# Performance work log

Hardware: AMD Instinct MI355X
Metric: run time of the kernel (lower is better)

Reference implementation:

```python
import jax, jax.numpy as jnp
import numpy as np

# MLABlock dims (from __init__ defaults / chosen init_kwargs)
B, S, D = 2, 2048, 2048
H = 16
NOPE, ROPE, VD = 128, 64, 128
KVR = 512
NE, TOPK = 12, 4
EI, SEI = 1024, 2048
THETA = 10000.0
MSCALE = 1.0
EPS = 1e-6


def setup_inputs() -> dict:
    key = jax.random.key(0)
    ks = jax.random.split(key, 14)
    w = lambda k, shp: jax.random.normal(k, shp, jnp.float32) * 0.02
    return {
        "x": jax.random.normal(ks[0], (B, S, D), jnp.float32),
        "start_pos": 0,
        "norm_w": jnp.ones((D,), jnp.float32),
        "wq": w(ks[1], (H * (NOPE + ROPE), D)),
        "wkv_a": w(ks[2], (KVR + ROPE, D)),
        "kv_norm_w": jnp.ones((KVR,), jnp.float32),
        "wkv_b": w(ks[3], (H * (NOPE + VD), KVR)),
        "wo": w(ks[4], (D, H * VD)),
        "gate_w": w(ks[5], (NE, D)),
        "gate_bias": w(ks[6], (NE,)),
        "w1": w(ks[7], (NE, EI, D)),
        "w2": w(ks[8], (NE, D, EI)),
        "w3": w(ks[9], (NE, EI, D)),
        "sw1": w(ks[10], (SEI, D)),
        "sw2": w(ks[11], (D, SEI)),
        "sw3": w(ks[12], (SEI, D)),
    }


def _rms(v, w):
    return v * jax.lax.rsqrt(jnp.mean(v * v, -1, keepdims=True) + EPS) * w


def reference(x, start_pos, norm_w, wq, wkv_a, kv_norm_w, wkv_b, wo,
              gate_w, gate_bias, w1, w2, w3, sw1, sw2, sw3):
    b, s, d = x.shape
    # ---- MLA attention sub-layer ----
    h = _rms(x, norm_w)
    q = (h @ wq.T).reshape(b, s, H, NOPE + ROPE)
    q_nope, q_pe = q[..., :NOPE], q[..., NOPE:]
    kv = h @ wkv_a.T                      # [b,s,KVR+ROPE]
    kv_lat, k_pe = kv[..., :KVR], kv[..., KVR:]
    # rotary embedding (interleaved pairs), positions start_pos..start_pos+s
    pos = jnp.arange(s, dtype=jnp.float32) + start_pos
    inv = 1.0 / (THETA ** (jnp.arange(0, ROPE, 2, dtype=jnp.float32) / ROPE))
    ang = pos[:, None] * inv              # [s, ROPE/2]
    cos = jnp.cos(ang)[None, :, None, :]
    sin = jnp.sin(ang)[None, :, None, :]
    def rot(t):                           # t: [b,s,h,ROPE]
        t1, t2 = t[..., 0::2], t[..., 1::2]
        return jnp.stack([t1 * cos - t2 * sin, t1 * sin + t2 * cos], -1).reshape(t.shape)
    q_pe = rot(q_pe)
    k_pe = rot(k_pe[:, :, None, :])       # [b,s,1,ROPE] shared across heads
    kv_lat = _rms(kv_lat, kv_norm_w)
    kvb = (kv_lat @ wkv_b.T).reshape(b, s, H, NOPE + VD)
    k_nope, v = kvb[..., :NOPE], kvb[..., NOPE:]
    k = jnp.concatenate([k_nope, jnp.broadcast_to(k_pe, (b, s, H, ROPE))], -1)
    qf = jnp.concatenate([q_nope, q_pe], -1)
    scale = MSCALE * (NOPE + ROPE) ** -0.5
    mask = jnp.triu(jnp.full((s, s), -1e9, x.dtype), 1)  # causal
    scores = jnp.einsum('bqhd,bkhd->bhqk', qf, k) * scale + mask
    attn = jax.nn.softmax(scores, -1)
    o = jnp.einsum('bhqk,bkhd->bqhd', attn, v).reshape(b, s, H * VD) @ wo.T
    first = o + x
    # ---- MoE sub-layer (shared self.norm reused) ----
    h2 = _rms(first, norm_w)
    g_scores = jax.nn.sigmoid(h2 @ gate_w.T)             # [b,s,NE]
    _, idx = jax.lax.top_k(g_scores + gate_bias, TOPK)   # adaptive-bias selection
    gw = jnp.take_along_axis(g_scores, idx, -1)          # weights from raw scores
    gw = gw / jnp.sum(gw, -1, keepdims=True)
    out = (jax.nn.silu(h2 @ sw1.T) * (h2 @ sw3.T)) @ sw2.T  # shared expert
    for e in range(NE):                                  # fixed small expert set
        we = jnp.sum(jnp.where(idx == e, gw, 0.0), -1)   # [b,s]
        ye = (jax.nn.silu(h2 @ w1[e].T) * (h2 @ w3[e].T)) @ w2[e].T
        out = out + we[..., None] * ye
    return out + first
```

## Files before the change

### kernel.cpp

```cpp
#include <hip/hip_runtime.h>
#include <cstdint>
#include <cstddef>
#include <cmath>

#define DI __device__ __forceinline__
typedef float f32x4 __attribute__((ext_vector_type(4)));
typedef __bf16 bf16x8 __attribute__((ext_vector_type(8)));
typedef unsigned short u16;
typedef unsigned int u32;

static constexpr int TKN = 4096, SEQ = 2048, DIM = 2048, NH = 16;

DI u16 f2bf(float f) {
  union { float f; u32 u; } v; v.f = f;
  u32 r = v.u + 0x7fffu + ((v.u >> 16) & 1u);
  return (u16)(r >> 16);
}
DI float bf2f(u16 h) {
  union { u32 u; float f; } v; v.u = ((u32)h) << 16;
  return v.f;
}
DI f32x4 mfma16(bf16x8 a, bf16x8 b, f32x4 c) {
  return __builtin_amdgcn_mfma_f32_16x16x32_bf16(a, b, c, 0, 0, 0);
}
DI void gld16(const u16* g, u16* l) {
  __builtin_amdgcn_global_load_lds((const __attribute__((address_space(1))) u32*)g,
                                   (__attribute__((address_space(3))) u32*)l, 16, 0, 0);
}

enum { EF_F32 = 0, EF_BF16 = 1, EF_RES = 2, EF_KV = 3, EF_SILU = 4, EF_ATOM = 5, EF_QROPE = 6 };
enum { AM_DIR = 0, AM_LIST = 1, AM_OFF = 2, AM_TIL = 3 };

template<int EPI, int AMODE, int NSEG>
__global__ __launch_bounds__(256)
void gemm_f(const u16* __restrict__ A, const u16* __restrict__ B, void* __restrict__ C,
            int M, int N, int K, size_t apl, size_t bpl,
            const int* __restrict__ list, const int* __restrict__ basep,
            const int* __restrict__ counts,
            const void* __restrict__ aux, const float* __restrict__ gws,
            u16* __restrict__ kd0, u16* __restrict__ kd1, u16* __restrict__ vT,
            const float* __restrict__ cosT, const int* __restrict__ tb)
{
  constexpr int BM = 128, BK = 64;
  __shared__ __align__(16) u16 As[BM * BK];
  __shared__ __align__(16) u16 Bs[BM * BK];
  int rowbase = 0;
  int m0, n0;
  if (AMODE == AM_TIL) {
    int ntile = N >> 7;
    int u = blockIdx.x / ntile;
    if (u >= tb[12]) return;
    n0 = (blockIdx.x - u * ntile) << 7;
    int e = 0;
    #pragma unroll
    for (int k = 0; k < 11; k++) if (tb[k + 1] <= u) e = k + 1;
    M = counts[e];
    rowbase = basep[e];
    m0 = (u - tb[e]) << 7;
    B += (size_t)e * (size_t)N * K;
  } else if (AMODE != AM_DIR) {
    int z = blockIdx.z;
    M = counts[z];
    rowbase = basep[z];
    B += (size_t)z * (size_t)N * K;
    m0 = blockIdx.x * BM; n0 = blockIdx.y * BM;
    if (m0 >= M) return;
  } else {
    m0 = blockIdx.x * BM; n0 = blockIdx.y * BM;
    if (m0 >= M) return;
  }
  int tid = threadIdx.x, lane = tid & 63, wid = tid >> 6;
  int wm = (wid >> 1) * 64, wn = (wid & 1) * 64;
  int lr = lane & 15, lk = (lane >> 4) * 8;

  const u16* asrc[4];
  const u16* bsrc[4];
  int l8 = lane >> 3, c8 = ((lane & 7) ^ l8) * 8;
  #pragma unroll
  for (int i = 0; i < 4; i++) {
    int chunk = wid * 4 + i;
    int ra = m0 + chunk * 8 + l8;
    size_t rowidx;
    if (AMODE == AM_LIST)      rowidx = (size_t)list[rowbase + (ra < M ? ra : 0)];
    else if (AMODE == AM_OFF || AMODE == AM_TIL)
                               rowidx = (size_t)(rowbase + (ra < M ? ra : 0));
    else                       rowidx = (size_t)ra;
    asrc[i] = A + rowidx * (size_t)K + c8;
    int rb = n0 + chunk * 8 + l8;
    if (rb >= N) rb = N - 1;
    bsrc[i] = B + (size_t)rb * K + c8;
  }

  f32x4 acc[4][4] = {};
  int sw = lr & 7;
  #pragma unroll 1
  for (int s = 0; s < NSEG; s++) {
    int sa = (s == 4) ? 2 : (s & 1);
    int sb = (s == 5) ? 2 : ((s >> 1) & 1);
    size_t ao = (size_t)sa * apl, bo = (size_t)sb * bpl;
    for (int kt = 0; kt < K; kt += BK) {
      #pragma unroll
      for (int i = 0; i < 4; i++) {
        gld16(asrc[i] + ao + kt, &As[(wid * 4 + i) * 512]);
        gld16(bsrc[i] + bo + kt, &Bs[(wid * 4 + i) * 512]);
      }
      __syncthreads();
      #pragma unroll
      for (int ko = 0; ko < BK; ko += 32) {
        bf16x8 af[4], bv[4];
        int sl = ((((ko + lk) >> 3) ^ sw) << 3);
        #pragma unroll
        for (int i = 0; i < 4; i++)
          af[i] = *(const bf16x8*)(&As[(wm + i * 16 + lr) * 64 + sl]);
        #pragma unroll
        for (int j = 0; j < 4; j++)
          bv[j] = *(const bf16x8*)(&Bs[(wn + j * 16 + lr) * 64 + sl]);
        #pragma unroll
        for (int i = 0; i < 4; i++)
          #pragma unroll
          for (int j = 0; j < 4; j++)
            acc[i][j] = mfma16(af[i], bv[j], acc[i][j]);
      }
      __syncthreads();
    }
  }

  int og = (lane >> 4) * 4;
  if (EPI == EF_KV) {
    if (((n0 >> 7) & 1) == 0) {
      #pragma unroll
      for (int i = 0; i < 4; i++)
        #pragma unroll
        for (int p = 0; p < 4; p++) {
          int r = m0 + wm + i * 16 + og + p;
          #pragma unroll
          for (int j = 0; j < 4; j++) {
            int c = n0 + wn + j * 16 + lr;
            float v = acc[i][j][p];
            int hd = c >> 8, cc = c & 127;
            u16 b0 = f2bf(v);
            u16 b1 = f2bf(v - bf2f(b0));
            size_t base = ((size_t)r * NH + hd) * 128 + cc;
            kd0[base] = b0; kd1[base] = b1;
          }
        }
    } else {
      constexpr size_t VPL = (size_t)32 * 128 * 2048;
      #pragma unroll
      for (int i = 0; i < 4; i++) {
        int r0 = m0 + wm + i * 16 + og;
        int bb = r0 >> 11, ss = r0 & 2047;
        #pragma unroll
        for (int j = 0; j < 4; j++) {
          int c = n0 + wn + j * 16 + lr;
          int hd = c >> 8, ccv = c & 127;
          ushort4 q0, q1, q2;
          #pragma unroll
          for (int p = 0; p < 4; p++) {
            float v = acc[i][j][p];
            u16 b0 = f2bf(v);
            float r1 = v - bf2f(b0);
            u16 b1 = f2bf(r1);
            u16 b2 = f2bf(r1 - bf2f(b1));
            ((u16*)&q0)[p] = b0; ((u16*)&q1)[p] = b1; ((u16*)&q2)[p] = b2;
          }
          size_t vb = ((size_t)((bb * 16 + hd) * 128 + ccv)) * 2048 + ss;
          *(ushort4*)(vT + vb) = q0;
          *(ushort4*)(vT + VPL + vb) = q1;
          *(ushort4*)(vT + 2 * VPL + vb) = q2;
        }
      }
    }
  } else {
    #pragma unroll
    for (int i = 0; i < 4; i++)
      #pragma unroll
      for (int p = 0; p < 4; p++) {
        int r = m0 + wm + i * 16 + og + p;
        if (EPI != EF_QROPE) { if (r >= M) continue; }
        size_t outr = (AMODE == AM_DIR) ? (size_t)r : (size_t)(rowbase + r);
        #pragma unroll
        for (int j = 0; j < 4; j++) {
          int c = n0 + wn + j * 16 + lr;
          float v = acc[i][j][p];
          if (EPI == EF_F32) {
            if (c < N) ((float*)C)[outr * N + c] = v;
          } else if (EPI == EF_BF16) {
            ((u16*)C)[outr * N + c] = f2bf(v);
          } else if (EPI == EF_RES) {
            ((float*)C)[outr * N + c] = v + ((const float*)aux)[outr * N + c];
          } else if (EPI == EF_SILU) {
            float t = bf2f(((const u16*)aux)[outr * N + c]);
            float sg = t / (1.f + __expf(-t));
            ((u16*)C)[outr * N + c] = f2bf(sg * v);
          } else if (EPI == EF_ATOM) {
            int tok = list[outr];
            float w = gws[outr];
            atomicAdd((float*)C + (size_t)tok * N + c, w * v);
          } else if (EPI == EF_QROPE) {
            int wi = c % 192;
            float vo = v;
            if (wi >= 128) {
              float part = __shfl_xor(v, 1);
              int jj = (wi - 128) >> 1;
              int srow = r & (SEQ - 1);
              float cs = cosT[srow * 32 + jj];
              float sn = ((const float*)aux)[srow * 32 + jj];
              vo = (c & 1) ? (part * sn + v * cs) : (v * cs - part * sn);
            }
            u16 b0 = f2bf(vo);
            u16 b1 = f2bf(vo - bf2f(b0));
            kd0[outr * (size_t)N + c] = b0;
            kd1[outr * (size_t)N + c] = b1;
          }
        }
      }
  }
}

__global__ __launch_bounds__(256)
void attn3(const u16* __restrict__ q0p, const u16* __restrict__ q1p,
           const u16* __restrict__ k0p, const u16* __restrict__ k1p,
           const u16* __restrict__ kp0, const u16* __restrict__ kp1,
           const u16* __restrict__ vT, u16* __restrict__ o0, float scale)
{
  constexpr int KLD = 200, VLD = 40, PLD = 36;
  constexpr size_t VPL = (size_t)32 * 128 * 2048;
  constexpr size_t OPL = (size_t)TKN * DIM;
  __shared__ __align__(16) u16 Ks[2][32 * KLD];
  __shared__ __align__(16) u16 Vt[3][128 * VLD];
  __shared__ __align__(16) float Ps[4][16 * PLD];

  int bh = blockIdx.y;
  int b = bh >> 4, h = bh & 15;
  int tid = threadIdx.x, lane = tid & 63, wid = tid >> 6;
  int lr = lane & 15, lg = lane >> 4, lk = lg * 8;
  size_t tbase = (size_t)b * SEQ;
  const u16* vbase = vT + (size_t)bh * 128 * 2048;

  for (int half = 0; half < 2; half++) {
    int qt = half ? (31 - (int)blockIdx.x) : (int)blockIdx.x;
    int q0r = qt * 64;
    bf16x8 qf[2][6];
    {
      size_t qoff = (tbase + q0r + wid * 16 + lr) * (size_t)3072 + h * 192;
      #pragma unroll
      for (int kc = 0; kc < 6; kc++) {
        qf[0][kc] = *(const bf16x8*)(q0p + qoff + kc * 32 + lk);
        qf[1][kc] = *(const bf16x8*)(q1p + qoff + kc * 32 + lk);
      }
    }
    f32x4 oacc[8] = {};
    float mrow[4], lrow[4];
    #pragma unroll
    for (int p = 0; p < 4; p++) { mrow[p] = -1e30f; lrow[p] = 0.f; }

    int nkt = 2 * qt + 2;
    for (int kt = 0; kt < nkt; kt++) {
      __syncthreads();
      int kr0 = kt * 32;
      #pragma unroll
      for (int p = 0; p < 2; p++) {
        const u16* knp = p ? k1p : k0p;
        const u16* kpp = p ? kp1 : kp0;
        #pragma unroll
        for (int i = 0; i < 2; i++) {
          int vv = tid + i * 256, r = vv >> 4, cc8 = (vv & 15) * 8;
          int4 d = *(const int4*)(knp + ((tbase + kr0 + r) * (size_t)NH + h) * 128 + cc8);
          *(int4*)(&Ks[p][r * KLD + cc8]) = d;
        }
        {
          int r = tid >> 3, cc8 = (tid & 7) * 8;
          int4 d = *(const int4*)(kpp + (tbase + kr0 + r) * (size_t)64 + cc8);
          *(int4*)(&Ks[p][r * KLD + 128 + cc8]) = d;
        }
      }
      #pragma unroll
      for (int p = 0; p < 3; p++) {
        #pragma unroll
        for (int i = 0; i < 2; i++) {
          int vv = tid + i * 256, d = vv >> 2, cc8 = (vv & 3) * 8;
          int4 dd = *(const int4*)(vbase + p * VPL + (size_t)d * 2048 + kr0 + cc8);
          *(int4*)(&Vt[p][d * VLD + cc8]) = dd;
        }
      }
      __syncthreads();

      f32x4 sacc[2] = {};
      #pragma unroll
      for (int j = 0; j < 2; j++)
        #pragma unroll
        for (int kc = 0; kc < 6; kc++) {
          bf16x8 kf0 = *(const bf16x8*)(&Ks[0][(j * 16 + lr) * KLD + kc * 32 + lk]);
          bf16x8 kf1 = *(const bf16x8*)(&Ks[1][(j * 16 + lr) * KLD + kc * 32 + lk]);
          f32x4 t = sacc[j];
          t = mfma16(qf[0][kc], kf0, t);
          t = mfma16(qf[1][kc], kf0, t);
          t = mfma16(qf[0][kc], kf1, t);
          sacc[j] = t;
        }

      bool tail = (kt >= 2 * qt);
      float fsc[4];
      #pragma unroll
      for (int p = 0; p < 4; p++) {
        float s0 = sacc[0][p] * scale, s1 = sacc[1][p] * scale;
        if (tail) {
          int qrow = q0r + wid * 16 + lg * 4 + p;
          if (kr0 + lr > qrow) s0 = -1e30f;
          if (kr0 + 16 + lr > qrow) s1 = -1e30f;
        }
        float mx = fmaxf(s0, s1);
        #pragma unroll
        for (int off = 1; off < 16; off <<= 1) mx = fmaxf(mx, __shfl_xor(mx, off));
        float mnew = fmaxf(mrow[p], mx);
        fsc[p] = __expf(mrow[p] - mnew);
        float e0 = __expf(s0 - mnew), e1 = __expf(s1 - mnew);
        float ssum = e0 + e1;
        #pragma unroll
        for (int off = 1; off < 16; off <<= 1) ssum += __shfl_xor(ssum, off);
        lrow[p] = lrow[p] * fsc[p] + ssum;
        mrow[p] = mnew;
        Ps[wid][(lg * 4 + p) * PLD + lr] = e0;
        Ps[wid][(lg * 4 + p) * PLD + 16 + lr] = e1;
      }
      #pragma unroll
      for (int jf = 0; jf < 8; jf++) {
        f32x4 t = oacc[jf];
        t[0] *= fsc[0]; t[1] *= fsc[1]; t[2] *= fsc[2]; t[3] *= fsc[3];
        oacc[jf] = t;
      }

      f32x4 pva = *(const f32x4*)(&Ps[wid][lr * PLD + lk]);
      f32x4 pvb = *(const f32x4*)(&Ps[wid][lr * PLD + lk + 4]);
      union { u16 us[8]; bf16x8 v; } pa0u, pa1u;
      #pragma unroll
      for (int e = 0; e < 4; e++) {
        float va = pva[e];
        u16 b0 = f2bf(va); pa0u.us[e] = b0; pa1u.us[e] = f2bf(va - bf2f(b0));
        float vb = pvb[e];
        u16 c0 = f2bf(vb); pa0u.us[4 + e] = c0; pa1u.us[4 + e] = f2bf(vb - bf2f(c0));
      }

      #pragma unroll
      for (int jf = 0; jf < 8; jf++) {
        bf16x8 vf0 = *(const bf16x8*)(&Vt[0][(jf * 16 + lr) * VLD + lk]);
        bf16x8 vf1 = *(const bf16x8*)(&Vt[1][(jf * 16 + lr) * VLD + lk]);
        bf16x8 vf2 = *(const bf16x8*)(&Vt[2][(jf * 16 + lr) * VLD + lk]);
        f32x4 t = oacc[jf];
        t = mfma16(pa0u.v, vf0, t);
        t = mfma16(pa1u.v, vf0, t);
        t = mfma16(pa0u.v, vf1, t);
        t = mfma16(pa1u.v, vf1, t);
        t = mfma16(pa0u.v, vf2, t);
        oacc[jf] = t;
      }
    }

    #pragma unroll
    for (int p = 0; p < 4; p++) {
      float inv = 1.f / lrow[p];
      int qrow = q0r + wid * 16 + lg * 4 + p;
      size_t base = (tbase + qrow) * (size_t)DIM + h * 128;
      #pragma unroll
      for (int jf = 0; jf < 8; jf++) {
        float val = oacc[jf][p] * inv;
        u16 b0 = f2bf(val);
        float r1 = val - bf2f(b0);
        u16 b1 = f2bf(r1);
        u16 b2 = f2bf(r1 - bf2f(b1));
        size_t idx = base + jf * 16 + lr;
        o0[idx] = b0; o0[OPL + idx] = b1; o0[2 * OPL + idx] = b2;
      }
    }
  }
}

__global__ __launch_bounds__(256)
void rmsnorm3(const float* __restrict__ x, const float* __restrict__ w, u16* __restrict__ out)
{
  __shared__ float sred[4];
  constexpr size_t PL = (size_t)TKN * DIM;
  int t = blockIdx.x, tid = threadIdx.x;
  const float* xp = x + (size_t)t * DIM;
  float vals[8], ss = 0.f;
  #pragma unroll
  for (int i = 0; i < 8; i++) { float v = xp[tid + i * 256]; vals[i] = v; ss += v * v; }
  #pragma unroll
  for (int off = 32; off > 0; off >>= 1) ss += __shfl_xor(ss, off);
  if ((tid & 63) == 0) sred[tid >> 6] = ss;
  __syncthreads();
  ss = sred[0] + sred[1] + sred[2] + sred[3];
  float rstd = 1.f / sqrtf(ss / (float)DIM + 1e-6f);
  #pragma unroll
  for (int i = 0; i < 8; i++) {
    int d = tid + i * 256;
    float v = vals[i] * rstd * w[d];
    u16 b0 = f2bf(v);
    float r1 = v - bf2f(b0);
    u16 b1 = f2bf(r1);
    u16 b2 = f2bf(r1 - bf2f(b1));
    size_t o = (size_t)t * DIM + d;
    out[o] = b0; out[PL + o] = b1; out[2 * PL + o] = b2;
  }
}

__global__ __launch_bounds__(256)
void split3(const float* __restrict__ src, u16* __restrict__ dst, size_t n, size_t pl)
{
  size_t i0 = ((size_t)blockIdx.x * 256 + threadIdx.x) * 4;
  size_t stride = (size_t)gridDim.x * 1024;
  for (size_t i = i0; i < n; i += stride) {
    float4 d = *(const float4*)(src + i);
    ushort4 b0, b1, b2; float r;
    b0.x = f2bf(d.x); r = d.x - bf2f(b0.x); b1.x = f2bf(r); b2.x = f2bf(r - bf2f(b1.x));
    b0.y = f2bf(d.y); r = d.y - bf2f(b0.y); b1.y = f2bf(r); b2.y = f2bf(r - bf2f(b1.y));
    b0.z = f2bf(d.z); r = d.z - bf2f(b0.z); b1.z = f2bf(r); b2.z = f2bf(r - bf2f(b1.z));
    b0.w = f2bf(d.w); r = d.w - bf2f(b0.w); b1.w = f2bf(r); b2.w = f2bf(r - bf2f(b1.w));
    *(ushort4*)(dst + i) = b0;
    *(ushort4*)(dst + pl + i) = b1;
    *(ushort4*)(dst + 2 * pl + i) = b2;
  }
}

__global__ __launch_bounds__(256)
void cvt1(const float* __restrict__ src, u16* __restrict__ dst, size_t n)
{
  size_t i0 = ((size_t)blockIdx.x * 256 + threadIdx.x) * 4;
  size_t stride = (size_t)gridDim.x * 1024;
  for (size_t i = i0; i < n; i += stride) {
    float4 d = *(const float4*)(src + i);
    ushort4 b;
    b.x = f2bf(d.x); b.y = f2bf(d.y); b.z = f2bf(d.z); b.w = f2bf(d.w);
    *(ushort4*)(dst + i) = b;
  }
}

__global__ __launch_bounds__(256)
void gather_h2(const u16* __restrict__ h2, const int* __restrict__ list,
               u16* __restrict__ h2g)
{
  int slot = blockIdx.x;
  int tok = list[slot];
  int4 d = *(const int4*)(h2 + (size_t)tok * DIM + threadIdx.x * 8);
  *(int4*)(h2g + (size_t)slot * DIM + threadIdx.x * 8) = d;
}

__global__ __launch_bounds__(256)
void kv_split(const float* __restrict__ kvraw, const float* __restrict__ kvw,
              u16* __restrict__ c0, u16* __restrict__ kp0, u16* __restrict__ kp1,
              const float* __restrict__ cosT, const float* __restrict__ sinT)
{
  __shared__ float sred[4];
  constexpr size_t CPL = (size_t)TKN * 512;
  int t = blockIdx.x, tid = threadIdx.x;
  const float* xp = kvraw + (size_t)t * 576;
  float v0 = xp[tid], v1 = xp[tid + 256];
  float ss = v0 * v0 + v1 * v1;
  #pragma unroll
  for (int off = 32; off > 0; off >>= 1) ss += __shfl_xor(ss, off);
  if ((tid & 63) == 0) sred[tid >> 6] = ss;
  __syncthreads();
  ss = sred[0] + sred[1] + sred[2] + sred[3];
  float rstd = 1.f / sqrtf(ss / 512.f + 1e-6f);
  #pragma unroll
  for (int half = 0; half < 2; half++) {
    float v = (half ? v1 : v0) * rstd * kvw[tid + half * 256];
    u16 b0 = f2bf(v);
    float r1 = v - bf2f(b0);
    u16 b1 = f2bf(r1);
    u16 b2 = f2bf(r1 - bf2f(b1));
    size_t o = (size_t)t * 512 + tid + half * 256;
    c0[o] = b0; c0[CPL + o] = b1; c0[2 * CPL + o] = b2;
  }
  if (tid < 32) {
    int srow = t & (SEQ - 1);
    float a = xp[512 + tid * 2], bb = xp[512 + tid * 2 + 1];
    float cs = cosT[srow * 32 + tid], sn = sinT[srow * 32 + tid];
    float ra = a * cs - bb * sn, rb = a * sn + bb * cs;
    u16 a0 = f2bf(ra), a1 = f2bf(ra - bf2f(a0));
    u16 c0b = f2bf(rb), c1 = f2bf(rb - bf2f(c0b));
    kp0[(size_t)t * 64 + tid * 2] = a0;     kp1[(size_t)t * 64 + tid * 2] = a1;
    kp0[(size_t)t * 64 + tid * 2 + 1] = c0b; kp1[(size_t)t * 64 + tid * 2 + 1] = c1;
  }
}

__global__ __launch_bounds__(256)
void rope_table(float* __restrict__ cosT, float* __restrict__ sinT, const int* __restrict__ sp)
{
  int i = blockIdx.x * 256 + threadIdx.x;
  if (i >= SEQ * 32) return;
  int j = i & 31, srow = i >> 5;
  float pos = (float)(srow + sp[0]);
  float inv = powf(10000.f, -(float)(2 * j) / 64.f);
  cosT[i] = cosf(pos * inv);
  sinT[i] = sinf(pos * inv);
}

__global__ __launch_bounds__(256)
void gate_topk(const float* __restrict__ first, const float* __restrict__ nw,
               const float* __restrict__ gwm, const float* __restrict__ gbias,
               int* __restrict__ idx, float* __restrict__ gw4, int* __restrict__ counts,
               u16* __restrict__ h2out)
{
  __shared__ float sred[4];
  __shared__ float sacc[12][4];
  int t = blockIdx.x, tid = threadIdx.x;
  const float* xp = first + (size_t)t * DIM;
  float vals[8], ss = 0.f;
  #pragma unroll
  for (int i = 0; i < 8; i++) { float v = xp[tid + i * 256]; vals[i] = v; ss += v * v; }
  #pragma unroll
  for (int off = 32; off > 0; off >>= 1) ss += __shfl_xor(ss, off);
  if ((tid & 63) == 0) sred[tid >> 6] = ss;
  __syncthreads();
  ss = sred[0] + sred[1] + sred[2] + sred[3];
  float rstd = 1.f / sqrtf(ss / (float)DIM + 1e-6f);
  float acc[12];
  #pragma unroll
  for (int e = 0; e < 12; e++) acc[e] = 0.f;
  #pragma unroll
  for (int i = 0; i < 8; i++) {
    int d = tid + i * 256;
    float v = vals[i] * rstd * nw[d];
    h2out[(size_t)t * DIM + d] = f2bf(v);
    #pragma unroll
    for (int e = 0; e < 12; e++) acc[e] += v * gwm[e * DIM + d];
  }
  #pragma unroll
  for (int e = 0; e < 12; e++) {
    float a = acc[e];
    #pragma unroll
    for (int off = 32; off > 0; off >>= 1) a += __shfl_xor(a, off);
    if ((tid & 63) == 0) sacc[e][tid >> 6] = a;
  }
  __syncthreads();
  if (tid == 0) {
    float g[12], sc[12];
    #pragma unroll
    for (int e = 0; e < 12; e++) {
      float s = sacc[e][0] + sacc[e][1] + sacc[e][2] + sacc[e][3];
      g[e] = 1.f / (1.f + __expf(-s));
      sc[e] = g[e] + gbias[e];
    }
    bool taken[12] = {};
    int sel[4];
    float wsum = 0.f;
    #pragma unroll
    for (int s4 = 0; s4 < 4; s4++) {
      float best = -1e38f; int bi = 0;
      for (int e = 0; e < 12; e++)
        if (!taken[e] && sc[e] > best) { best = sc[e]; bi = e; }
      taken[bi] = true; sel[s4] = bi; wsum += g[bi];
    }
    #pragma unroll
    for (int s4 = 0; s4 < 4; s4++) {
      idx[t * 4 + s4] = sel[s4];
      gw4[t * 4 + s4] = g[sel[s4]] / wsum;
      atomicAdd(&counts[sel[s4]], 1);
    }
  }
}

__global__ void prefix12(const int* __restrict__ counts, int* __restrict__ basep,
                         int* __restrict__ cursor, int* __restrict__ tb)
{
  if (threadIdx.x == 0) {
    int run = 0, trun = 0;
    for (int e = 0; e < 12; e++) {
      basep[e] = run; tb[e] = trun;
      run += counts[e];
      trun += (counts[e] + 127) >> 7;
      cursor[e] = 0;
    }
    tb[12] = trun;
  }
}

__global__ __launch_bounds__(256)
void fill_lists(const int* __restrict__ idx, const int* __restrict__ basep,
                int* __restrict__ cursor, int* __restrict__ list,
                const float* __restrict__ gw4, float* __restrict__ gws)
{
  int t = blockIdx.x * 256 + threadIdx.x;
  if (t >= TKN) return;
  #pragma unroll
  for (int s = 0; s < 4; s++) {
    int e = idx[t * 4 + s];
    int pos = atomicAdd(&cursor[e], 1);
    list[basep[e] + pos] = t;
    gws[basep[e] + pos] = gw4[t * 4 + s];
  }
}

extern "C" void kernel_launch(void* const* d_in, const int* in_sizes, int n_in,
                              void* d_out, int out_size, void* d_ws, size_t ws_size,
                              hipStream_t stream)
{
  (void)in_sizes; (void)n_in; (void)out_size; (void)ws_size;
  const float* x      = (const float*)d_in[0];
  const int*   sp     = (const int*)d_in[1];
  const float* norm_w = (const float*)d_in[2];
  const float* wq     = (const float*)d_in[3];
  const float* wkv_a  = (const float*)d_in[4];
  const float* kvnw   = (const float*)d_in[5];
  const float* wkv_b  = (const float*)d_in[6];
  const float* wo     = (const float*)d_in[7];
  const float* gatew  = (const float*)d_in[8];
  const float* gateb  = (const float*)d_in[9];
  const float* w1     = (const float*)d_in[10];
  const float* w2     = (const float*)d_in[11];
  const float* w3     = (const float*)d_in[12];
  const float* sw1    = (const float*)d_in[13];
  const float* sw2    = (const float*)d_in[14];
  const float* sw3    = (const float*)d_in[15];
  float* out = (float*)d_out;
  char* ws = (char*)d_ws;

  const size_t D0 = 0, D1 = 50331648ull, D2 = 100663296ull, D3 = 150994944ull;
  const size_t SM = 188743680ull;
  u16* hpl   = (u16*)(ws + D0);
  u16* cpl   = (u16*)(ws + D0);
  u16* wkvbp = (u16*)(ws + D0 + 12582912ull);
  u16* opl   = (u16*)(ws + D0);
  u16* t1b   = (u16*)(ws + D0);
  u16* asb   = (u16*)(ws + D0 + 16777216ull);
  u16* qpl   = (u16*)(ws + D1);
  u16* swp   = (u16*)(ws + D1 + 25165824ull);
  u16* vtp   = (u16*)(ws + D2);
  float* firstb = (float*)(ws + D2);
  u16* h2b   = (u16*)(ws + D2 + 33554432ull);
  u16* wqp   = (u16*)(ws + D3);
  u16* wkvap = (u16*)(ws + D3);
  float* kvr = (float*)(ws + D3 + 7077888ull);
  u16* kpl0  = (u16*)(ws + D3);
  u16* kpl1  = kpl0 + 8388608ull;
  u16* kpe0  = (u16*)(ws + D3 + 33554432ull);
  u16* kpe1  = kpe0 + 262144ull;
  u16* wop   = (u16*)(ws + D3);
  u16* h2g   = (u16*)(ws + 0);
  u16* y1e   = (u16*)(ws + 67108864ull);
  u16* aee   = (u16*)(ws + 100663296ull);
  u16* wexp  = (u16*)(ws + 134217728ull);
  float* cosT = (float*)(ws + SM);
  float* sinT = (float*)(ws + SM + 262144ull);
  int*   idxb = (int*)(ws + SM + 524288ull);
  float* gw4b = (float*)(ws + SM + 589824ull);
  int*   listb= (int*)(ws + SM + 655360ull);
  float* gwsb = (float*)(ws + SM + 720896ull);
  int*   cntb = (int*)(ws + SM + 786432ull);
  int*   curb = (int*)(ws + SM + 786688ull);
  int*   baseb= (int*)(ws + SM + 786944ull);
  int*   tbb  = (int*)(ws + SM + 787200ull);

  const size_t PL_TD = (size_t)TKN * DIM;

  hipMemsetAsync(cntb, 0, 256, stream);
  rope_table<<<dim3(256), 256, 0, stream>>>(cosT, sinT, sp);
  rmsnorm3<<<dim3(TKN), 256, 0, stream>>>(x, norm_w, hpl);

  split3<<<dim3(1024), 256, 0, stream>>>(wq, wqp, (size_t)3072 * 2048, 6291456ull);
  gemm_f<EF_QROPE, AM_DIR, 3><<<dim3(32, 24), 256, 0, stream>>>(
      hpl, wqp, nullptr, TKN, 3072, 2048, PL_TD, 6291456ull,
      nullptr, nullptr, nullptr, sinT, nullptr, qpl, qpl + 12582912ull, nullptr, cosT, nullptr);

  split3<<<dim3(512), 256, 0, stream>>>(wkv_a, wkvap, (size_t)576 * 2048, 1179648ull);
  gemm_f<EF_F32, AM_DIR, 6><<<dim3(32, 5), 256, 0, stream>>>(
      hpl, wkvap, kvr, TKN, 576, 2048, PL_TD, 1179648ull,
      nullptr, nullptr, nullptr, nullptr, nullptr, nullptr, nullptr, nullptr, nullptr, nullptr);

  kv_split<<<dim3(TKN), 256, 0, stream>>>(kvr, kvnw, cpl, kpe0, kpe1, cosT, sinT);

  split3<<<dim3(1024), 256, 0, stream>>>(wkv_b, wkvbp, (size_t)4096 * 512, 2097152ull);
  gemm_f<EF_KV, AM_DIR, 6><<<dim3(32, 32), 256, 0, stream>>>(
      cpl, wkvbp, nullptr, TKN, 4096, 512, 2097152ull, 2097152ull,
      nullptr, nullptr, nullptr, nullptr, nullptr, kpl0, kpl1, vtp, nullptr, nullptr);

  attn3<<<dim3(16, 32), 256, 0, stream>>>(qpl, qpl + 12582912ull, kpl0, kpl1,
      kpe0, kpe1, vtp, opl, 1.f / sqrtf(192.f));

  split3<<<dim3(1024), 256, 0, stream>>>(wo, wop, (size_t)2048 * 2048, 4194304ull);
  gemm_f<EF_RES, AM_DIR, 6><<<dim3(32, 16), 256, 0, stream>>>(
      opl, wop, firstb, TKN, 2048, 2048, PL_TD, 4194304ull,
      nullptr, nullptr, nullptr, x, nullptr, nullptr, nullptr, nullptr, nullptr, nullptr);

  gate_topk<<<dim3(TKN), 256, 0, stream>>>(firstb, norm_w, gatew, gateb, idxb, gw4b, cntb, h2b);
  prefix12<<<dim3(1), 64, 0, stream>>>(cntb, baseb, curb, tbb);
  fill_lists<<<dim3(16), 256, 0, stream>>>(idxb, baseb, curb, listb, gw4b, gwsb);

  cvt1<<<dim3(1024), 256, 0, stream>>>(sw1, swp, (size_t)2048 * 2048);
  cvt1<<<dim3(1024), 256, 0, stream>>>(sw3, swp + 4194304ull, (size_t)2048 * 2048);
  cvt1<<<dim3(1024), 256, 0, stream>>>(sw2, swp + 8388608ull, (size_t)2048 * 2048);
  gemm_f<EF_BF16, AM_DIR, 1><<<dim3(32, 16), 256, 0, stream>>>(
      h2b, swp, t1b, TKN, 2048, 2048, 0, 0,
      nullptr, nullptr, nullptr, nullptr, nullptr, nullptr, nullptr, nullptr, nullptr, nullptr);
  gemm_f<EF_SILU, AM_DIR, 1><<<dim3(32, 16), 256, 0, stream>>>(
      h2b, swp + 4194304ull, asb, TKN, 2048, 2048, 0, 0,
      nullptr, nullptr, nullptr, t1b, nullptr, nullptr, nullptr, nullptr, nullptr, nullptr);
  gemm_f<EF_RES, AM_DIR, 1><<<dim3(32, 16), 256, 0, stream>>>(
      asb, swp + 8388608ull, out, TKN, 2048, 2048, 0, 0,
      nullptr, nullptr, nullptr, firstb, nullptr, nullptr, nullptr, nullptr, nullptr, nullptr);

  gather_h2<<<dim3(TKN * 4), 256, 0, stream>>>(h2b, listb, h2g);
  cvt1<<<dim3(2048), 256, 0, stream>>>(w1, wexp, (size_t)12 * 1024 * 2048);
  gemm_f<EF_BF16, AM_TIL, 1><<<dim3(12 * 32 * 8), 256, 0, stream>>>(
      h2g, wexp, y1e, 0, 1024, 2048, 0, 0,
      listb, baseb, cntb, nullptr, nullptr, nullptr, nullptr, nullptr, nullptr, tbb);
  cvt1<<<dim3(2048), 256, 0, stream>>>(w3, wexp, (size_t)12 * 1024 * 2048);
  gemm_f<EF_SILU, AM_TIL, 1><<<dim3(12 * 32 * 8), 256, 0, stream>>>(
      h2g, wexp, aee, 0, 1024, 2048, 0, 0,
      listb, baseb, cntb, y1e, nullptr, nullptr, nullptr, nullptr, nullptr, tbb);
  cvt1<<<dim3(2048), 256, 0, stream>>>(w2, wexp, (size_t)12 * 2048 * 1024);
  gemm_f<EF_ATOM, AM_TIL, 1><<<dim3(12 * 32 * 16), 256, 0, stream>>>(
      aee, wexp, out, 0, 2048, 1024, 0, 0,
      listb, baseb, cntb, nullptr, gwsb, nullptr, nullptr, nullptr, nullptr, tbb);
}
```

Measured before the change: 2.021 ms.

## Replace atomic scatter-add in expert down-projection with bf16 store and gather-combine kernel

The last expert GEMM no longer scatters weighted results into the output with float atomicAdd. It now writes per-slot bf16 rows to a workspace buffer. A new final_combine kernel uses a token-to-slot map built in fill_lists to gather each token's four expert rows, weight them and add them to the output. This removes atomic contention and scattered read-modify-write traffic, at the cost of an extra 32 MB bf16 intermediate, an extra launch, and rounding expert outputs to bf16 before combining.

```diff
diff --git a/kernel.cpp b/kernel.cpp
--- a/kernel.cpp
+++ b/kernel.cpp
@@ -28,7 +28,7 @@
                                    (__attribute__((address_space(3))) u32*)l, 16, 0, 0);
 }
 
-enum { EF_F32 = 0, EF_BF16 = 1, EF_RES = 2, EF_KV = 3, EF_SILU = 4, EF_ATOM = 5, EF_QROPE = 6 };
+enum { EF_F32 = 0, EF_BF16 = 1, EF_RES = 2, EF_KV = 3, EF_SILU = 4, EF_QROPE = 6 };
 enum { AM_DIR = 0, AM_LIST = 1, AM_OFF = 2, AM_TIL = 3 };
 
 template<int EPI, int AMODE, int NSEG>
@@ -193,10 +193,6 @@
             float t = bf2f(((const u16*)aux)[outr * N + c]);
             float sg = t / (1.f + __expf(-t));
             ((u16*)C)[outr * N + c] = f2bf(sg * v);
-          } else if (EPI == EF_ATOM) {
-            int tok = list[outr];
-            float w = gws[outr];
-            atomicAdd((float*)C + (size_t)tok * N + c, w * v);
           } else if (EPI == EF_QROPE) {
             int wi = c % 192;
             float vo = v;
@@ -447,6 +443,25 @@
 }
 
 __global__ __launch_bounds__(256)
+void final_combine(float* __restrict__ out, const u16* __restrict__ yout,
+                   const float* __restrict__ gw4, const int* __restrict__ slotrow)
+{
+  int t = blockIdx.x, tid = threadIdx.x;
+  int r0 = slotrow[t * 4], r1 = slotrow[t * 4 + 1];
+  int r2 = slotrow[t * 4 + 2], r3 = slotrow[t * 4 + 3];
+  float w0 = gw4[t * 4], w1_ = gw4[t * 4 + 1], w2_ = gw4[t * 4 + 2], w3_ = gw4[t * 4 + 3];
+  #pragma unroll
+  for (int i = 0; i < 8; i++) {
+    int d = tid + i * 256;
+    size_t o = (size_t)t * DIM + d;
+    out[o] += w0 * bf2f(yout[(size_t)r0 * DIM + d])
+            + w1_ * bf2f(yout[(size_t)r1 * DIM + d])
+            + w2_ * bf2f(yout[(size_t)r2 * DIM + d])
+            + w3_ * bf2f(yout[(size_t)r3 * DIM + d]);
+  }
+}
+
+__global__ __launch_bounds__(256)
 void kv_split(const float* __restrict__ kvraw, const float* __restrict__ kvw,
               u16* __restrict__ c0, u16* __restrict__ kp0, u16* __restrict__ kp1,
               const float* __restrict__ cosT, const float* __restrict__ sinT)
@@ -580,7 +595,8 @@
 __global__ __launch_bounds__(256)
 void fill_lists(const int* __restrict__ idx, const int* __restrict__ basep,
                 int* __restrict__ cursor, int* __restrict__ list,
-                const float* __restrict__ gw4, float* __restrict__ gws)
+                const float* __restrict__ gw4, float* __restrict__ gws,
+                int* __restrict__ slotrow)
 {
   int t = blockIdx.x * 256 + threadIdx.x;
   if (t >= TKN) return;
@@ -590,6 +606,7 @@
     int pos = atomicAdd(&cursor[e], 1);
     list[basep[e] + pos] = t;
     gws[basep[e] + pos] = gw4[t * 4 + s];
+    slotrow[t * 4 + s] = basep[e] + pos;
   }
 }
 
@@ -639,6 +656,7 @@
   u16* kpe1  = kpe0 + 262144ull;
   u16* wop   = (u16*)(ws + D3);
   u16* h2g   = (u16*)(ws + 0);
+  u16* yout  = (u16*)(ws + 0);
   u16* y1e   = (u16*)(ws + 67108864ull);
   u16* aee   = (u16*)(ws + 100663296ull);
   u16* wexp  = (u16*)(ws + 134217728ull);
@@ -652,6 +670,7 @@
   int*   curb = (int*)(ws + SM + 786688ull);
   int*   baseb= (int*)(ws + SM + 786944ull);
   int*   tbb  = (int*)(ws + SM + 787200ull);
+  int*   slotb= (int*)(ws + SM + 787456ull);
 
   const size_t PL_TD = (size_t)TKN * DIM;
 
@@ -686,7 +705,7 @@
 
   gate_topk<<<dim3(TKN), 256, 0, stream>>>(firstb, norm_w, gatew, gateb, idxb, gw4b, cntb, h2b);
   prefix12<<<dim3(1), 64, 0, stream>>>(cntb, baseb, curb, tbb);
-  fill_lists<<<dim3(16), 256, 0, stream>>>(idxb, baseb, curb, listb, gw4b, gwsb);
+  fill_lists<<<dim3(16), 256, 0, stream>>>(idxb, baseb, curb, listb, gw4b, gwsb, slotb);
 
   cvt1<<<dim3(1024), 256, 0, stream>>>(sw1, swp, (size_t)2048 * 2048);
   cvt1<<<dim3(1024), 256, 0, stream>>>(sw3, swp + 4194304ull, (size_t)2048 * 2048);
@@ -711,7 +730,8 @@
       h2g, wexp, aee, 0, 1024, 2048, 0, 0,
       listb, baseb, cntb, y1e, nullptr, nullptr, nullptr, nullptr, nullptr, tbb);
   cvt1<<<dim3(2048), 256, 0, stream>>>(w2, wexp, (size_t)12 * 2048 * 1024);
-  gemm_f<EF_ATOM, AM_TIL, 1><<<dim3(12 * 32 * 16), 256, 0, stream>>>(
-      aee, wexp, out, 0, 2048, 1024, 0, 0,
-      listb, baseb, cntb, nullptr, gwsb, nullptr, nullptr, nullptr, nullptr, tbb);
-}
+  gemm_f<EF_BF16, AM_TIL, 1><<<dim3(12 * 32 * 16), 256, 0, stream>>>(
+      aee, wexp, yout, 0, 2048, 1024, 0, 0,
+      listb, baseb, cntb, nullptr, nullptr, nullptr, nullptr, nullptr, nullptr, tbb);
+  final_combine<<<dim3(TKN), 256, 0, stream>>>(out, yout, gw4b, slotb);
+}
```

Measured after the change: 1.981 ms, median of 2. 2.0% less time.
